# Performance work log

Hardware: AMD Instinct MI355X
Metric: run time of the kernel (lower is better)

The kernel has to match this reference:

```python
import jax, jax.numpy as jnp
import numpy as np

WIN = 7          # window_size
DIM = 192        # embedding dim
HEADS = 6
HEAD_DIM = DIM // HEADS
B_ = 4096        # batch * num_windows
N = WIN * WIN    # tokens per window


def _relative_position_index():
    coords = np.stack(np.meshgrid(np.arange(WIN), np.arange(WIN), indexing='ij'))  # [2,7,7]
    flat = coords.reshape(2, -1)                                                   # [2,49]
    rel = flat[:, :, None] - flat[:, None, :]                                      # [2,49,49]
    rel = rel.transpose(1, 2, 0).astype(np.int32)                                  # [49,49,2]
    rel[:, :, 0] += WIN - 1
    rel[:, :, 1] += WIN - 1
    rel[:, :, 0] *= 2 * WIN - 1
    return jnp.asarray(rel.sum(-1), dtype=jnp.int32)                               # [49,49]


def setup_inputs() -> dict:
    key = jax.random.key(0)
    ks = jax.random.split(key, 6)
    std = 0.02
    return {
        'x': jax.random.normal(ks[0], (B_, N, DIM), dtype=jnp.float32),
        'qkv_w': jax.random.normal(ks[1], (3 * DIM, DIM), dtype=jnp.float32) * std,
        'qkv_b': jnp.zeros((3 * DIM,), dtype=jnp.float32),
        'proj_w': jax.random.normal(ks[2], (DIM, DIM), dtype=jnp.float32) * std,
        'proj_b': jnp.zeros((DIM,), dtype=jnp.float32),
        'bias_table': jax.random.normal(ks[3], ((2 * WIN - 1) ** 2, HEADS), dtype=jnp.float32) * std,
        'rel_index': _relative_position_index(),
    }


def reference(x, qkv_w, qkv_b, proj_w, proj_b, bias_table, rel_index):
    B, n, C = x.shape
    # qkv projection -> [3, B, H, N, hd]
    qkv = (x @ qkv_w.T + qkv_b).reshape(B, n, 3, HEADS, HEAD_DIM)
    qkv = jnp.transpose(qkv, (2, 0, 3, 1, 4))
    q, k, v = qkv[0], qkv[1], qkv[2]
    # relative position bias: [H, N, N]
    bias = bias_table[rel_index.reshape(-1)].reshape(n, n, HEADS)
    bias = jnp.transpose(bias, (2, 0, 1))[None]  # [1, H, N, N]
    scale = 1.0 / jnp.sqrt(jnp.asarray(HEAD_DIM, dtype=x.dtype))
    logits = jnp.einsum('bhnd,bhmd->bhnm', q, k) * scale + bias
    attn = jax.nn.softmax(logits, axis=-1)
    out = jnp.einsum('bhnm,bhmd->bhnd', attn, v)
    out = jnp.transpose(out, (0, 2, 1, 3)).reshape(B, n, C)
    return out @ proj_w.T + proj_b
```

## Files before the change

kernel.cpp:

```cpp
#include <hip/hip_runtime.h>

#define NTOK 49
#define DIM 192
#define HEADS 6

typedef __bf16 bf16x8 __attribute__((ext_vector_type(8)));
typedef float f32x4 __attribute__((ext_vector_type(4)));
typedef unsigned int u32x2 __attribute__((ext_vector_type(2)));
typedef short s16x4 __attribute__((ext_vector_type(4)));

#define WPROJ_USH 110592
#define BIAS_BYTE 294912

#define SCALE  0.17677669529663687f
#define LOG2E  1.4426950408889634f
#define SCALEQ (SCALE * LOG2E)

#define OUT_WIN_BYTES 37632

__device__ __forceinline__ unsigned int pack2(float a, float b) {
    unsigned short lo = __builtin_bit_cast(unsigned short, (__bf16)a);
    unsigned short hi = __builtin_bit_cast(unsigned short, (__bf16)b);
    return (unsigned int)lo | ((unsigned int)hi << 16);
}

__device__ __forceinline__ f32x4 mfma32(int4 a, int4 b, f32x4 c) {
    return __builtin_amdgcn_mfma_f32_16x16x32_bf16(
        __builtin_bit_cast(bf16x8, a), __builtin_bit_cast(bf16x8, b), c, 0, 0, 0);
}

#if __has_builtin(__builtin_amdgcn_mfma_f32_16x16x16bf16_1k)
__device__ __forceinline__ f32x4 mfma16(u32x2 a, u32x2 b, f32x4 c) {
    return __builtin_amdgcn_mfma_f32_16x16x16bf16_1k(
        __builtin_bit_cast(s16x4, a), __builtin_bit_cast(s16x4, b), c, 0, 0, 0);
}
#else
__device__ __forceinline__ f32x4 mfma16(u32x2 a, u32x2 b, f32x4 c) {
    f32x4 d;
    asm volatile("s_nop 1\n\t"
                 "v_mfma_f32_16x16x16_bf16 %0, %1, %2, %3\n\t"
                 "s_nop 7\n\t"
                 "s_nop 7"
                 : "=v"(d) : "v"(a), "v"(b), "0"(c));
    return d;
}
#endif

#if __has_builtin(__builtin_amdgcn_exp2f)
__device__ __forceinline__ float exp2_fast(float x) { return __builtin_amdgcn_exp2f(x); }
#else
__device__ __forceinline__ float exp2_fast(float x) { return exp2f(x); }
#endif

__global__ void prep(const float* __restrict__ qkv_w, const float* __restrict__ proj_w,
                     const float* __restrict__ bias_table, const int* __restrict__ rel_index,
                     unsigned short* __restrict__ w16, float* __restrict__ bias_cd) {
    int bid = blockIdx.x;
    if (bid < 72) {
        int c = bid * 256 + threadIdx.x;
        if (c < 13824) {
            int lane = c & 63;
            int t = c >> 6;
            int ot = t % 36, ks = t / 36;
            int f  = ot * 16 + (lane & 15);
            int k0 = ks * 32 + (lane >> 4) * 8;
            float sc = (f < 192) ? SCALEQ : 1.0f;
            const float* p = qkv_w + (size_t)f * DIM + k0;
            float4 a = *(const float4*)p;
            float4 b = *(const float4*)(p + 4);
            uint4 o;
            o.x = pack2(a.x * sc, a.y * sc); o.y = pack2(a.z * sc, a.w * sc);
            o.z = pack2(b.x * sc, b.y * sc); o.w = pack2(b.z * sc, b.w * sc);
            *(uint4*)(w16 + (size_t)c * 8) = o;
        } else {
            int cc = c - 13824;
            int line = cc >> 5;
            int pair = cc & 31;
            int ks = line / 12, ot = line % 12;
            unsigned int w[4];
            #pragma unroll
            for (int s = 0; s < 2; ++s) {
                int lane = pair * 2 + s;
                int q = lane >> 4, ci = lane & 15;
                const float* p = proj_w + (size_t)(ot*16 + ci) * DIM + ks*16 + q*4;
                float4 a = *(const float4*)p;
                w[s*2 + 0] = pack2(a.x, a.y);
                w[s*2 + 1] = pack2(a.z, a.w);
            }
            uint4 o = {w[0], w[1], w[2], w[3]};
            *(uint4*)(w16 + WPROJ_USH + (size_t)cc * 8) = o;
        }
    } else {
        int gid = (bid - 72) * 256 + threadIdx.x;
        int lane = gid & 63;
        int tile = (gid >> 6) & 15;
        int h    = gid >> 10;
        int kt = tile >> 2, qt = tile & 3;
        int qtok = qt * 16 + (lane & 15);
        int key0 = kt * 16 + (lane >> 4) * 4;
        float4 v;
        float* vp = (float*)&v;
        for (int r = 0; r < 4; ++r) {
            int key = key0 + r;
            float val;
            if (key >= NTOK)       val = -1e30f;
            else if (qtok >= NTOK) val = 0.0f;
            else                   val = bias_table[rel_index[qtok * NTOK + key] * HEADS + h] * LOG2E;
            vp[r] = val;
        }
        *(float4*)(bias_cd + (size_t)gid * 4) = v;
    }
}

#define K1_LDS 24576

__global__ __launch_bounds__(192, 2) void win_attn(
    const float* __restrict__ x,
    const float* __restrict__ qkv_b,
    const unsigned short* __restrict__ wq16,
    const float* __restrict__ bias_cd,
    float* __restrict__ outO)
{
    extern __shared__ char smem[];
    const int tid  = threadIdx.x;
    const int lane = tid & 63;
    const int wv   = tid >> 6;
    const int widx = blockIdx.x;
    const int l15  = lane & 15;
    const int quad = lane >> 4;

    #pragma unroll
    for (int i = 0; i < 8; ++i) {
        int c  = tid + i * 192;
        int cl = c & 63;
        int mt = (c >> 6) & 3;
        int ks = c >> 8;
        int tok = mt * 16 + (cl & 15);
        int d0  = ks * 32 + (cl >> 4) * 8;
        uint4 o = {0u, 0u, 0u, 0u};
        if (tok < NTOK) {
            const float* p = x + ((size_t)widx * NTOK + tok) * DIM + d0;
            float4 a  = *(const float4*)p;
            float4 bb = *(const float4*)(p + 4);
            o.x = pack2(a.x, a.y); o.y = pack2(a.z, a.w);
            o.z = pack2(bb.x, bb.y); o.w = pack2(bb.z, bb.w);
        }
        *(uint4*)(smem + (size_t)c * 16) = o;
    }
    __syncthreads();

    char* const xrd = smem + lane * 16;

    #pragma unroll 1
    for (int hi = 0; hi < 2; ++hi) {
        const int h = wv + hi * 3;
        const unsigned short* const wqh = wq16 + (size_t)(h * 128 + lane) * 8;
        const float* const bcb = bias_cd + (size_t)(h * 1024 + lane) * 4;

        u32x2 qb[2][4], kb[2][4];
        {
            f32x4 qa[2][4], ka[2][4];
            #pragma unroll
            for (int ft = 0; ft < 2; ++ft)
                #pragma unroll
                for (int nt = 0; nt < 4; ++nt) { qa[ft][nt] = (f32x4){0,0,0,0}; ka[ft][nt] = (f32x4){0,0,0,0}; }
            #pragma unroll 2
            for (int ks = 0; ks < 6; ++ks) {
                int4 wq[2], wk[2];
                #pragma unroll
                for (int ft = 0; ft < 2; ++ft) {
                    wq[ft] = *(const int4*)(wqh + (ks*36 + ft) * 512);
                    wk[ft] = *(const int4*)(wqh + (ks*36 + ft) * 512 + 6144);
                }
                #pragma unroll
                for (int nt = 0; nt < 4; ++nt) {
                    int4 xf = *(const int4*)(xrd + (ks*4 + nt) * 1024);
                    #pragma unroll
                    for (int ft = 0; ft < 2; ++ft) {
                        qa[ft][nt] = mfma32(wq[ft], xf, qa[ft][nt]);
                        ka[ft][nt] = mfma32(wk[ft], xf, ka[ft][nt]);
                    }
                }
            }
            #pragma unroll
            for (int ft = 0; ft < 2; ++ft) {
                float4 tq = *(const float4*)(qkv_b + (h*2 + ft)*16 + quad*4);
                float4 tk = *(const float4*)(qkv_b + 192 + (h*2 + ft)*16 + quad*4);
                #pragma unroll
                for (int nt = 0; nt < 4; ++nt) {
                    qb[ft][nt] = (u32x2){ pack2(qa[ft][nt][0] + tq.x*SCALEQ, qa[ft][nt][1] + tq.y*SCALEQ),
                                          pack2(qa[ft][nt][2] + tq.z*SCALEQ, qa[ft][nt][3] + tq.w*SCALEQ) };
                    kb[ft][nt] = (u32x2){ pack2(ka[ft][nt][0] + tk.x, ka[ft][nt][1] + tk.y),
                                          pack2(ka[ft][nt][2] + tk.z, ka[ft][nt][3] + tk.w) };
                }
            }
        }

        u32x2 vb[4][2];
        {
            f32x4 va[4][2];
            #pragma unroll
            for (int mt = 0; mt < 4; ++mt)
                #pragma unroll
                for (int nv = 0; nv < 2; ++nv) va[mt][nv] = (f32x4){0,0,0,0};
            #pragma unroll 2
            for (int ks = 0; ks < 6; ++ks) {
                int4 wvv[2];
                #pragma unroll
                for (int nv = 0; nv < 2; ++nv)
                    wvv[nv] = *(const int4*)(wqh + (ks*36 + nv) * 512 + 12288);
                #pragma unroll
                for (int mt = 0; mt < 4; ++mt) {
                    int4 xf = *(const int4*)(xrd + (ks*4 + mt) * 1024);
                    #pragma unroll
                    for (int nv = 0; nv < 2; ++nv)
                        va[mt][nv] = mfma32(xf, wvv[nv], va[mt][nv]);
                }
            }
            const float bv0 = qkv_b[384 + h*32 + l15];
            const float bv1 = qkv_b[384 + h*32 + 16 + l15];
            #pragma unroll
            for (int mt = 0; mt < 4; ++mt) {
                vb[mt][0] = (u32x2){ pack2(va[mt][0][0] + bv0, va[mt][0][1] + bv0),
                                     pack2(va[mt][0][2] + bv0, va[mt][0][3] + bv0) };
                vb[mt][1] = (u32x2){ pack2(va[mt][1][0] + bv1, va[mt][1][1] + bv1),
                                     pack2(va[mt][1][2] + bv1, va[mt][1][3] + bv1) };
            }
        }

        char* const og = (char*)outO + (size_t)widx * OUT_WIN_BYTES;
        #pragma unroll 2
        for (int qt = 0; qt < 4; ++qt) {
            float sum = 0.f;
            u32x2 pq[4];
            #pragma unroll
            for (int kt = 0; kt < 4; ++kt) {
                f32x4 s = (f32x4){0,0,0,0};
                s = mfma16(kb[0][kt], qb[0][qt], s);
                s = mfma16(kb[1][kt], qb[1][qt], s);
                float4 bc = *(const float4*)(bcb + (kt*4 + qt) * 256);
                float e0 = exp2_fast(s[0] + bc.x);
                float e1 = exp2_fast(s[1] + bc.y);
                float e2 = exp2_fast(s[2] + bc.z);
                float e3 = exp2_fast(s[3] + bc.w);
                sum += (e0 + e1) + (e2 + e3);
                pq[kt] = (u32x2){ pack2(e0, e1), pack2(e2, e3) };
            }
            sum += __shfl_xor(sum, 16);
            sum += __shfl_xor(sum, 32);
            const float invq = 1.0f / sum;

            f32x4 o0 = (f32x4){0,0,0,0}, o1 = (f32x4){0,0,0,0};
            #pragma unroll
            for (int kt = 0; kt < 4; ++kt) {
                o0 = mfma16(vb[kt][0], pq[kt], o0);
                o1 = mfma16(vb[kt][1], pq[kt], o1);
            }
            u32x2 ow0 = (u32x2){ pack2(o0[0]*invq, o0[1]*invq), pack2(o0[2]*invq, o0[3]*invq) };
            u32x2 ow1 = (u32x2){ pack2(o1[0]*invq, o1[1]*invq), pack2(o1[2]*invq, o1[3]*invq) };
            *(u32x2*)(og + (size_t)(((h*2 + 0)*4 + qt) * 512) + lane * 8) = ow0;
            *(u32x2*)(og + (size_t)(((h*2 + 1)*4 + qt) * 512) + lane * 8) = ow1;
        }
    }
}

#define K2_LDS 24576

__global__ __launch_bounds__(384, 4) void proj_k(
    float* __restrict__ out,
    const unsigned short* __restrict__ wp16,
    const float* __restrict__ proj_b)
{
    extern __shared__ char smem[];
    const int tid  = threadIdx.x;
    const int lane = tid & 63;
    const int h    = tid >> 6;
    const int l15  = lane & 15;
    const int quad = lane >> 4;
    const int widx = blockIdx.x;

    char* const base = (char*)out + (size_t)widx * OUT_WIN_BYTES;
    #pragma unroll
    for (int i = 0; i < 4; ++i) {
        int c = tid + i * 384;
        *(uint4*)(smem + (size_t)c * 16) = *(const uint4*)(base + (size_t)c * 16);
    }
    __syncthreads();

    char* const ard = smem + lane * 8;
    const char* const wpb = (const char*)wp16 + lane * 8;

    f32x4 acc[4][2];
    #pragma unroll
    for (int mt = 0; mt < 4; ++mt)
        #pragma unroll
        for (int j = 0; j < 2; ++j) acc[mt][j] = (f32x4){0, 0, 0, 0};
    #pragma unroll 3
    for (int ks = 0; ks < 12; ++ks) {
        u32x2 wb[2];
        #pragma unroll
        for (int j = 0; j < 2; ++j)
            wb[j] = *(const u32x2*)(wpb + (size_t)((ks*12 + h*2 + j) * 512));
        #pragma unroll
        for (int mt = 0; mt < 4; ++mt) {
            u32x2 oa = *(const u32x2*)(ard + (ks*4 + mt) * 512);
            #pragma unroll
            for (int j = 0; j < 2; ++j)
                acc[mt][j] = mfma16(oa, wb[j], acc[mt][j]);
        }
    }
    #pragma unroll
    for (int j = 0; j < 2; ++j) {
        const int o = (h*2 + j) * 16 + l15;
        const float pb = proj_b[o];
        #pragma unroll
        for (int mt = 0; mt < 4; ++mt) {
            const int t0 = mt * 16 + quad * 4;
            #pragma unroll
            for (int r = 0; r < 4; ++r) {
                const int t = t0 + r;
                if (t < NTOK)
                    out[((size_t)widx * NTOK + t) * DIM + o] = acc[mt][j][r] + pb;
            }
        }
    }
}

extern "C" void kernel_launch(void* const* d_in, const int* in_sizes, int n_in,
                              void* d_out, int out_size, void* d_ws, size_t ws_size,
                              hipStream_t stream) {
    const float* x          = (const float*)d_in[0];
    const float* qkv_w      = (const float*)d_in[1];
    const float* qkv_b      = (const float*)d_in[2];
    const float* proj_w     = (const float*)d_in[3];
    const float* proj_b     = (const float*)d_in[4];
    const float* bias_table = (const float*)d_in[5];
    const int*   rel_index  = (const int*)d_in[6];
    float* out = (float*)d_out;

    unsigned short* w16 = (unsigned short*)d_ws;
    float* bias_cd = (float*)((char*)d_ws + BIAS_BYTE);

    prep<<<96, 256, 0, stream>>>(qkv_w, proj_w, bias_table, rel_index, w16, bias_cd);

    (void)hipFuncSetAttribute((const void*)win_attn,
                              hipFuncAttributeMaxDynamicSharedMemorySize, K1_LDS);
    win_attn<<<4096, 192, K1_LDS, stream>>>(x, qkv_b, w16, bias_cd, out);

    (void)hipFuncSetAttribute((const void*)proj_k,
                              hipFuncAttributeMaxDynamicSharedMemorySize, K2_LDS);
    proj_k<<<4096, 384, K2_LDS, stream>>>(out, w16 + WPROJ_USH, proj_b);
}
```

Baseline: 402.0 us.

## Fuse output projection into attention kernel via LDS staging

The attention output is staged in shared memory instead of global memory, and the projection GEMM runs in the same kernel after a barrier, removing the second kernel launch and the round trip of the intermediate through HBM. Each of the three waves now computes four output column tiles instead of two, and LDS per block doubles. This may reduce occupancy, and the larger accumulator array adds register pressure.

```diff
diff --git a/kernel.cpp b/kernel.cpp
--- a/kernel.cpp
+++ b/kernel.cpp
@@ -15,8 +15,6 @@
 #define SCALE  0.17677669529663687f
 #define LOG2E  1.4426950408889634f
 #define SCALEQ (SCALE * LOG2E)
-
-#define OUT_WIN_BYTES 37632
 
 __device__ __forceinline__ unsigned int pack2(float a, float b) {
     unsigned short lo = __builtin_bit_cast(unsigned short, (__bf16)a);
@@ -112,14 +110,17 @@
     }
 }
 
-#define K1_LDS 24576
+#define O_OFF  24576
+#define K1_LDS 49152
 
 __global__ __launch_bounds__(192, 2) void win_attn(
     const float* __restrict__ x,
     const float* __restrict__ qkv_b,
+    const float* __restrict__ proj_b,
     const unsigned short* __restrict__ wq16,
+    const unsigned short* __restrict__ wp16,
     const float* __restrict__ bias_cd,
-    float* __restrict__ outO)
+    float* __restrict__ out)
 {
     extern __shared__ char smem[];
     const int tid  = threadIdx.x;
@@ -228,7 +229,7 @@
             }
         }
 
-        char* const og = (char*)outO + (size_t)widx * OUT_WIN_BYTES;
+        char* const olds = smem + O_OFF + lane * 8;
         #pragma unroll 2
         for (int qt = 0; qt < 4; ++qt) {
             float sum = 0.f;
@@ -258,69 +259,48 @@
             }
             u32x2 ow0 = (u32x2){ pack2(o0[0]*invq, o0[1]*invq), pack2(o0[2]*invq, o0[3]*invq) };
             u32x2 ow1 = (u32x2){ pack2(o1[0]*invq, o1[1]*invq), pack2(o1[2]*invq, o1[3]*invq) };
-            *(u32x2*)(og + (size_t)(((h*2 + 0)*4 + qt) * 512) + lane * 8) = ow0;
-            *(u32x2*)(og + (size_t)(((h*2 + 1)*4 + qt) * 512) + lane * 8) = ow1;
-        }
-    }
-}
-
-#define K2_LDS 24576
-
-__global__ __launch_bounds__(384, 4) void proj_k(
-    float* __restrict__ out,
-    const unsigned short* __restrict__ wp16,
-    const float* __restrict__ proj_b)
-{
-    extern __shared__ char smem[];
-    const int tid  = threadIdx.x;
-    const int lane = tid & 63;
-    const int h    = tid >> 6;
-    const int l15  = lane & 15;
-    const int quad = lane >> 4;
-    const int widx = blockIdx.x;
-
-    char* const base = (char*)out + (size_t)widx * OUT_WIN_BYTES;
-    #pragma unroll
-    for (int i = 0; i < 4; ++i) {
-        int c = tid + i * 384;
-        *(uint4*)(smem + (size_t)c * 16) = *(const uint4*)(base + (size_t)c * 16);
+            *(u32x2*)(olds + (size_t)(((h*2 + 0)*4 + qt) * 512)) = ow0;
+            *(u32x2*)(olds + (size_t)(((h*2 + 1)*4 + qt) * 512)) = ow1;
+        }
     }
     __syncthreads();
 
-    char* const ard = smem + lane * 8;
-    const char* const wpb = (const char*)wp16 + lane * 8;
-
-    f32x4 acc[4][2];
-    #pragma unroll
-    for (int mt = 0; mt < 4; ++mt)
+    {
+        char* const ord = smem + O_OFF + lane * 8;
+        const char* const wpb = (const char*)wp16 + lane * 8;
+
+        f32x4 acc[4][4];
         #pragma unroll
-        for (int j = 0; j < 2; ++j) acc[mt][j] = (f32x4){0, 0, 0, 0};
-    #pragma unroll 3
-    for (int ks = 0; ks < 12; ++ks) {
-        u32x2 wb[2];
+        for (int mt = 0; mt < 4; ++mt)
+            #pragma unroll
+            for (int j = 0; j < 4; ++j) acc[mt][j] = (f32x4){0, 0, 0, 0};
+        #pragma unroll 3
+        for (int ks = 0; ks < 12; ++ks) {
+            u32x2 wb[4];
+            #pragma unroll
+            for (int j = 0; j < 4; ++j)
+                wb[j] = *(const u32x2*)(wpb + (size_t)((ks*12 + wv*4 + j) * 512));
+            #pragma unroll
+            for (int mt = 0; mt < 4; ++mt) {
+                u32x2 oa = *(const u32x2*)(ord + (ks*4 + mt) * 512);
+                #pragma unroll
+                for (int j = 0; j < 4; ++j)
+                    acc[mt][j] = mfma16(oa, wb[j], acc[mt][j]);
+            }
+        }
         #pragma unroll
-        for (int j = 0; j < 2; ++j)
-            wb[j] = *(const u32x2*)(wpb + (size_t)((ks*12 + h*2 + j) * 512));
-        #pragma unroll
-        for (int mt = 0; mt < 4; ++mt) {
-            u32x2 oa = *(const u32x2*)(ard + (ks*4 + mt) * 512);
-            #pragma unroll
-            for (int j = 0; j < 2; ++j)
-                acc[mt][j] = mfma16(oa, wb[j], acc[mt][j]);
-        }
-    }
-    #pragma unroll
-    for (int j = 0; j < 2; ++j) {
-        const int o = (h*2 + j) * 16 + l15;
-        const float pb = proj_b[o];
-        #pragma unroll
-        for (int mt = 0; mt < 4; ++mt) {
-            const int t0 = mt * 16 + quad * 4;
-            #pragma unroll
-            for (int r = 0; r < 4; ++r) {
-                const int t = t0 + r;
-                if (t < NTOK)
-                    out[((size_t)widx * NTOK + t) * DIM + o] = acc[mt][j][r] + pb;
+        for (int j = 0; j < 4; ++j) {
+            const int o = (wv*4 + j) * 16 + l15;
+            const float pb = proj_b[o];
+            #pragma unroll
+            for (int mt = 0; mt < 4; ++mt) {
+                const int t0 = mt * 16 + quad * 4;
+                #pragma unroll
+                for (int r = 0; r < 4; ++r) {
+                    const int t = t0 + r;
+                    if (t < NTOK)
+                        out[((size_t)widx * NTOK + t) * DIM + o] = acc[mt][j][r] + pb;
+                }
             }
         }
     }
@@ -345,9 +325,6 @@
 
     (void)hipFuncSetAttribute((const void*)win_attn,
                               hipFuncAttributeMaxDynamicSharedMemorySize, K1_LDS);
-    win_attn<<<4096, 192, K1_LDS, stream>>>(x, qkv_b, w16, bias_cd, out);
-
-    (void)hipFuncSetAttribute((const void*)proj_k,
-                              hipFuncAttributeMaxDynamicSharedMemorySize, K2_LDS);
-    proj_k<<<4096, 384, K2_LDS, stream>>>(out, w16 + WPROJ_USH, proj_b);
-}
+    win_attn<<<4096, 192, K1_LDS, stream>>>(x, qkv_b, proj_b,
+                                            w16, w16 + WPROJ_USH, bias_cd, out);
+}
```

Result: no change. 401.3 us (-0.2%).
